# Optimization experiments

Measured on AMD Instinct MI355X. Metric: run time of the kernel, lower is better.

Reference implementation:

```python
import jax, jax.numpy as jnp
import numpy as np
import math

N, E, IN, OUT, H = 50000, 200000, 128, 128, 4
EPS = 1e-5
NEG_SLOPE = 0.01


def _ln(a):
    m = jnp.mean(a, axis=-1, keepdims=True)
    v = jnp.mean((a - m) ** 2, axis=-1, keepdims=True)
    return (a - m) / jnp.sqrt(v + EPS)


def setup_inputs() -> dict:
    key = jax.random.key(0)
    ks = jax.random.split(key, 24)
    glorot = lambda k, shape: jax.random.uniform(k, shape, jnp.float32,
                                                 -math.sqrt(6.0 / (shape[-2] + shape[-1])),
                                                 math.sqrt(6.0 / (shape[-2] + shape[-1])))
    lin = lambda k, fan_in, shape: jax.random.uniform(k, shape, jnp.float32,
                                                      -1.0 / math.sqrt(fan_in), 1.0 / math.sqrt(fan_in))
    inp = {
        "x": jax.random.normal(ks[0], (N, IN), jnp.float32),
        "edge_index": jax.random.randint(ks[1], (2, E), 0, N, jnp.int32),
        "edge_feature": jax.random.normal(ks[2], (E, IN), jnp.float32),
        # per-head projection matrices [H, IN, OUT]
        "Kv2v": glorot(ks[3], (H, IN, OUT)),
        "Ke2v": glorot(ks[4], (H, IN, OUT)),
        "Vv2v": glorot(ks[5], (H, IN, OUT)),
        "Ve2v": glorot(ks[6], (H, IN, OUT)),
        # per-head linear_update: [H, 2*OUT, 2*OUT]
        "lu_W": lin(ks[7], 2 * OUT, (H, 2 * OUT, 2 * OUT)),
        "lu_b": lin(ks[8], 2 * OUT, (H, 2 * OUT)),
        "ln1_g": jnp.ones((H, 2 * OUT), jnp.float32),
        "ln1_b": jnp.zeros((H, 2 * OUT), jnp.float32),
        # per-head msg_layer linear: [H, 2*OUT, OUT]
        "msg_W": lin(ks[9], 2 * OUT, (H, 2 * OUT, OUT)),
        "msg_b": lin(ks[10], 2 * OUT, (H, OUT)),
        "ln2_g": jnp.ones((H, OUT), jnp.float32),
        "ln2_b": jnp.zeros((H, OUT), jnp.float32),
        # concat projection [OUT*H, OUT]
        "cat_W": lin(ks[11], OUT * H, (OUT * H, OUT)),
        "cat_b": lin(ks[12], OUT * H, (OUT,)),
        # input projection [IN, OUT]
        "inp_W": lin(ks[13], IN, (IN, OUT)),
        "inp_b": lin(ks[14], IN, (OUT,)),
        # batchnorm affine
        "bn_g": jnp.ones((OUT,), jnp.float32),
        "bn_b": jnp.zeros((OUT,), jnp.float32),
    }
    return inp


def reference(x, edge_index, edge_feature, Kv2v, Ke2v, Vv2v, Ve2v,
              lu_W, lu_b, ln1_g, ln1_b, msg_W, msg_b, ln2_g, ln2_b,
              cat_W, cat_b, inp_W, inp_b, bn_g, bn_b):
    src, dst = edge_index[0], edge_index[1]  # j -> i
    scale = 1.0 / math.sqrt(2 * OUT)
    heads = []
    for h in range(H):  # small fixed loop over structurally distinct heads
        Kv = x @ Kv2v[h]            # [N, OUT]
        Vv = x @ Vv2v[h]
        KE = edge_feature @ Ke2v[h]  # [E, OUT]
        VE = edge_feature @ Ve2v[h]
        q_i = Kv[dst]                # [E, OUT]
        query = jnp.concatenate([q_i, q_i], axis=1)          # [E, 2*OUT]
        key_j = jnp.concatenate([Kv[src], KE], axis=1)       # [E, 2*OUT]
        alpha = query * key_j * scale
        val = jnp.concatenate([Vv[src], VE], axis=1)         # [E, 2*OUT]
        gate = jax.nn.sigmoid(_ln(alpha) * ln1_g[h] + ln1_b[h])
        m = (val @ lu_W[h] + lu_b[h]) * gate                 # [E, 2*OUT]
        m = m @ msg_W[h] + msg_b[h]                          # [E, OUT]
        m = _ln(m) * ln2_g[h] + ln2_b[h]
        m = jax.nn.leaky_relu(m, NEG_SLOPE)
        heads.append(jax.ops.segment_sum(m, dst, num_segments=N))  # [N, OUT]
    hv = jnp.concatenate(heads, axis=1)          # [N, OUT*H]
    out = hv @ cat_W + cat_b                      # [N, OUT]
    mu = jnp.mean(out, axis=0)
    var = jnp.mean((out - mu) ** 2, axis=0)      # biased, training-mode BN
    out = (out - mu) / jnp.sqrt(var + EPS) * bn_g + bn_b
    out = jax.nn.leaky_relu(out, NEG_SLOPE)
    return out + (x @ inp_W + inp_b)
```

## Files before the change

### kernel.cpp

```cpp
#include <hip/hip_runtime.h>
#include <hip/hip_bf16.h>

#define NN 50000
#define NE 200000
#define HEADS 4
#define EPSV 1e-5f
#define NEGS 0.01f

using f32x4 = __attribute__((ext_vector_type(4))) float;
using s16x8 = __attribute__((ext_vector_type(8))) short;
using bf16x8 = __attribute__((ext_vector_type(8))) __bf16;

__device__ __forceinline__ short f2bf(float f) {
    union { float f; unsigned u; } v; v.f = f;
    unsigned r = v.u + 0x7FFFu + ((v.u >> 16) & 1u);
    return (short)(r >> 16);
}
__device__ __forceinline__ float bf2f(short s) {
    union { unsigned u; float f; } v; v.u = ((unsigned)(unsigned short)s) << 16;
    return v.f;
}
__device__ __forceinline__ f32x4 mfma16(s16x8 a, s16x8 b, f32x4 c) {
    return __builtin_amdgcn_mfma_f32_16x16x32_bf16(
        __builtin_bit_cast(bf16x8, a), __builtin_bit_cast(bf16x8, b), c, 0, 0, 0);
}
__device__ __forceinline__ void gld16(const void* g, void* l) {
    __builtin_amdgcn_global_load_lds(
        (const __attribute__((address_space(1))) void*)g,
        (__attribute__((address_space(3))) void*)l, 16, 0, 0);
}
__device__ __forceinline__ void dma8(const short* src, char* dst, int w, int lane) {
    gld16(src + w * 512 + lane * 8,        dst + w * 1024);
    gld16(src + 2048 + w * 512 + lane * 8, dst + 4096 + w * 1024);
}

__global__ void prep_weights(const float* __restrict__ Kv2v, const float* __restrict__ Vv2v,
                             const float* __restrict__ inpW,
                             const float* __restrict__ Ke2v, const float* __restrict__ Ve2v,
                             const float* __restrict__ luW, const float* __restrict__ msgW,
                             const float* __restrict__ catW,
                             short* __restrict__ nodeW_t, short* __restrict__ imgW)
{
    int i = blockIdx.x * 256 + threadIdx.x;
    if (i < 147456) {
        int j = i >> 7, k = i & 127;
        float v;
        if (j < 512)       v = Kv2v[(j >> 7) * 16384 + k * 128 + (j & 127)];
        else if (j < 1024) v = Vv2v[((j - 512) >> 7) * 16384 + k * 128 + (j & 127)];
        else               v = inpW[k * 128 + (j - 1024)];
        nodeW_t[i] = f2bf(v);
        return;
    }
    i -= 147456;
    if (i >= 589824) return;
    int h = i / 147456;
    int r = i % 147456;
    short* img = imgW + h * 147456;
    if (r < 16384) {
        int colc = r >> 7, k = r & 127;
        img[(colc * 128 + k) ^ ((colc & 7) << 3)] = f2bf(Ke2v[h * 16384 + k * 128 + colc]);
    } else if (r < 32768) {
        int e = r - 16384; int colc = e >> 7, k = e & 127;
        img[16384 + ((colc * 128 + k) ^ ((colc & 7) << 3))] = f2bf(Ve2v[h * 16384 + k * 128 + colc]);
    } else if (r < 98304) {
        int e = r - 32768; int c = e >> 14, ec = e & 16383;
        int colc = ec >> 8, k = ec & 255; int col = c * 64 + colc;
        img[32768 + c * 16384 + ((colc * 256 + k) ^ ((colc & 7) << 3))] =
            f2bf(luW[h * 65536 + k * 256 + col]);
    } else if (r < 131072) {
        int e = r - 98304; int c = e >> 14, ec = e & 16383;
        int colc = ec >> 8, k = ec & 255; int col = c * 64 + colc;
        img[98304 + c * 16384 + ((colc * 256 + k) ^ ((colc & 7) << 3))] =
            f2bf(msgW[h * 32768 + k * 128 + col]);
    } else {
        int e = r - 131072; int colc = e >> 7, k = e & 127;
        img[131072 + ((colc * 128 + k) ^ ((colc & 7) << 3))] =
            f2bf(catW[(h * 128 + k) * 128 + colc]);
    }
}

__global__ __launch_bounds__(256, 2)
void node_proj(const float* __restrict__ x, const short* __restrict__ nodeW_t,
               short* __restrict__ Kv_all, short* __restrict__ Vv_all,
               float* __restrict__ resid)
{
    __shared__ alignas(16) short xt[64 * 128];
    const int tid = threadIdx.x;
    const int row0 = blockIdx.x * 64;
    #pragma unroll
    for (int it = 0; it < 8; ++it) {
        int idx4 = it * 256 + tid;
        int r = idx4 >> 5;
        int c = (idx4 & 31) * 4;
        float4 v = {0.f, 0.f, 0.f, 0.f};
        if (row0 + r < NN) v = *(const float4*)(x + (size_t)(row0 + r) * 128 + c);
        short4 sw; sw.x = f2bf(v.x); sw.y = f2bf(v.y); sw.z = f2bf(v.z); sw.w = f2bf(v.w);
        int byte = (r * 256 + c * 2) ^ ((r & 7) << 4);
        *(short4*)((char*)xt + byte) = sw;
    }
    __syncthreads();
    const int lane = tid & 63, w = tid >> 6;
    const int l15 = lane & 15, lg = lane >> 4;
    const int rloc = w * 16 + l15;
    s16x8 a[4];
    #pragma unroll
    for (int ks = 0; ks < 4; ++ks) {
        int byte = (rloc * 256 + (ks * 32 + lg * 8) * 2) ^ ((rloc & 7) << 4);
        a[ks] = *(const s16x8*)((const char*)xt + byte);
    }
    const int rowC = row0 + w * 16 + lg * 4;
    for (int nc = 0; nc < 18; ++nc) {
        f32x4 acc[4];
        s16x8 b[16];
        #pragma unroll
        for (int q = 0; q < 4; ++q) {
            acc[q] = (f32x4){0.f, 0.f, 0.f, 0.f};
            int j = (nc * 4 + q) * 16 + l15;
            #pragma unroll
            for (int ks = 0; ks < 4; ++ks)
                b[q * 4 + ks] = *(const s16x8*)(nodeW_t + j * 128 + ks * 32 + lg * 8);
        }
        #pragma unroll
        for (int q = 0; q < 4; ++q)
            #pragma unroll
            for (int ks = 0; ks < 4; ++ks)
                acc[q] = mfma16(a[ks], b[q * 4 + ks], acc[q]);
        #pragma unroll
        for (int q = 0; q < 4; ++q) {
            int j = (nc * 4 + q) * 16 + l15;
            #pragma unroll
            for (int r = 0; r < 4; ++r) {
                int row = rowC + r;
                if (row >= NN) continue;
                if (j < 512)       Kv_all[(size_t)row * 512 + j] = f2bf(acc[q][r]);
                else if (j < 1024) Vv_all[(size_t)row * 512 + (j - 512)] = f2bf(acc[q][r]);
                else               resid[(size_t)row * 128 + (j - 1024)] = acc[q][r];
            }
        }
    }
}

#define B128h(buf, ct, ks) \
    (*(const s16x8*)((const short*)(buf) + (((((ct) * 16 + l15) * 128) + (ks) * 32 + lg * 8) ^ ((l15 & 7) << 3))))
#define B256h(buf, ks) \
    (*(const s16x8*)((const short*)(buf) + ((l15 * 256 + (ks) * 32 + lg * 8) ^ ((l15 & 7) << 3))))
#define WAITV(N) asm volatile("s_waitcnt vmcnt(" #N ")" ::: "memory")
#define SBAR() do { __builtin_amdgcn_s_barrier(); __builtin_amdgcn_sched_barrier(0); } while (0)
#define PRIO1() __builtin_amdgcn_s_setprio(1)
#define PRIO0() __builtin_amdgcn_s_setprio(0)

__global__ __launch_bounds__(256, 1)
void edge_kernel(const float* __restrict__ ef, const int* __restrict__ eidx,
                 const short* __restrict__ Kv_all, const short* __restrict__ Vv_all,
                 const short* __restrict__ imgW,
                 const float* __restrict__ lu_b, const float* __restrict__ ln1_g,
                 const float* __restrict__ ln1_b, const float* __restrict__ msg_b,
                 const float* __restrict__ ln2_g, const float* __restrict__ ln2_b,
                 float* __restrict__ out1)
{
    extern __shared__ char lds[];
    const int tid = threadIdx.x;
    const int lane = tid & 63, w = tid >> 6;
    const int l15 = lane & 15, lg = lane >> 4;
    const int e0 = blockIdx.x * 64 + w * 16;
    const int rb = lg * 4;
    char* myscr = lds + 32768 + w * 12288;
    float* bls = (float*)(lds + 81920);
    const float scale = 0.0625f;

    {
        int j = tid;
        #pragma unroll
        for (int it = 0; it < 4; ++it, j += 256) {
            bls[j] = ln1_g[j]; bls[1024 + j] = ln1_b[j]; bls[2048 + j] = lu_b[j];
        }
        if (tid < 256) {
            bls[3072 + tid] = msg_b[tid];       bls[3072 + 256 + tid] = msg_b[256 + tid];
            bls[3584 + tid] = ln2_g[tid];       bls[3584 + 256 + tid] = ln2_g[256 + tid];
            bls[4096 + tid] = ln2_b[tid];       bls[4096 + 256 + tid] = ln2_b[256 + tid];
        }
        asm volatile("s_waitcnt lgkmcnt(0)" ::: "memory");
    }

    const float* efr = ef + (size_t)(e0 + l15) * 128 + lg * 8;
    s16x8 aef[4];
    #pragma unroll
    for (int ks = 0; ks < 4; ++ks) {
        float4 v0 = *(const float4*)(efr + ks * 32);
        float4 v1 = *(const float4*)(efr + ks * 32 + 4);
        s16x8 t;
        t[0] = f2bf(v0.x); t[1] = f2bf(v0.y); t[2] = f2bf(v0.z); t[3] = f2bf(v0.w);
        t[4] = f2bf(v1.x); t[5] = f2bf(v1.y); t[6] = f2bf(v1.z); t[7] = f2bf(v1.w);
        aef[ks] = t;
    }
    const int srcA = eidx[e0 + l15];
    int dstC[4];
    #pragma unroll
    for (int r = 0; r < 4; ++r) dstC[r] = eidx[NE + e0 + rb + r];
    const int gRow = lane >> 2;
    const int gChunk = lane & 3;
    const int dstG = eidx[NE + e0 + gRow];
    const int srcG = eidx[e0 + gRow];

    dma8(imgW,        lds,         w, lane);
    dma8(imgW + 4096, lds + 8192,  w, lane);
    dma8(imgW + 8192, lds + 16384, w, lane);

    f32x4 outc[8];
    #pragma unroll
    for (int nt = 0; nt < 8; ++nt) outc[nt] = (f32x4){0.f, 0.f, 0.f, 0.f};

    for (int h = 0; h < HEADS; ++h) {
        const short* hb = imgW + h * 147456;
        f32x4 accK[8];
        #pragma unroll
        for (int nt = 0; nt < 8; ++nt) accK[nt] = (f32x4){0, 0, 0, 0};
        s16x8 vvr[4];
        unsigned gpk[16][2];

        #pragma unroll
        for (int p = 0; p < 4; ++p) {
            WAITV(4); SBAR();
            dma8(hb + (p + 3) * 4096, lds + ((p + 3) & 3) * 8192, w, lane);
            const char* bA = lds + (p & 3) * 8192;
            PRIO1();
            #pragma unroll
            for (int ks = 0; ks < 4; ++ks) {
                accK[p * 2]     = mfma16(aef[ks], B128h(bA, 0, ks), accK[p * 2]);
                accK[p * 2 + 1] = mfma16(aef[ks], B128h(bA, 1, ks), accK[p * 2 + 1]);
            }
            PRIO0();
            if (p == 0) {
                #pragma unroll
                for (int j = 0; j < 4; ++j) {
                    s16x8 qv = *(const s16x8*)(Kv_all + (size_t)dstG * 512 + h * 128 + gChunk * 32 + j * 8);
                    s16x8 kv = *(const s16x8*)(Kv_all + (size_t)srcG * 512 + h * 128 + gChunk * 32 + j * 8);
                    int byte = gRow * 256 + ((((gChunk * 4 + j) * 16)) ^ ((gRow & 7) << 4));
                    *(s16x8*)(myscr + byte) = qv;
                    *(s16x8*)(myscr + 4096 + byte) = kv;
                }
            }
        }

        #pragma unroll
        for (int i = 0; i < 4; ++i) {
            const int p = 4 + i;
            WAITV(4); SBAR();
            dma8(hb + (p + 3) * 4096, lds + ((p + 3) & 3) * 8192, w, lane);
            const char* bA = lds + (p & 3) * 8192;
            f32x4 aV0 = (f32x4){0, 0, 0, 0}, aV1 = (f32x4){0, 0, 0, 0};
            PRIO1();
            #pragma unroll
            for (int ks = 0; ks < 4; ++ks) {
                aV0 = mfma16(aef[ks], B128h(bA, 0, ks), aV0);
                aV1 = mfma16(aef[ks], B128h(bA, 1, ks), aV1);
            }
            PRIO0();
            #pragma unroll
            for (int t = 0; t < 2; ++t) {
                f32x4 av = t ? aV1 : aV0;
                int c = (i * 2 + t) * 16 + l15;
                #pragma unroll
                for (int r = 0; r < 4; ++r) {
                    int row = rb + r;
                    int byte = 8192 + ((row * 256 + c * 2) ^ ((row & 7) << 4));
                    *(short*)(myscr + byte) = f2bf(av[r]);
                }
            }
            if (i == 0) {
                #pragma unroll
                for (int ks = 0; ks < 4; ++ks)
                    vvr[ks] = *(const s16x8*)(Vv_all + (size_t)srcA * 512 + h * 128 + ks * 32 + lg * 8);
            }
            if (i == 3) {
                #pragma unroll
                for (int r = 0; r < 4; ++r) {
                    const int i2r = rb + r;
                    const int swz = (i2r & 7) << 4;
                    float al[16];
                    float s = 0.f, s2 = 0.f;
                    #pragma unroll
                    for (int nt = 0; nt < 8; ++nt) {
                        int off = (i2r * 256 + nt * 32 + l15 * 2) ^ swz;
                        float q  = bf2f(*(const short*)(myscr + off));
                        float k1 = bf2f(*(const short*)(myscr + 4096 + off));
                        float alo = q * k1 * scale;
                        float ahi = q * accK[nt][r] * scale;
                        al[nt] = alo; al[nt + 8] = ahi;
                        s += alo + ahi; s2 += alo * alo + ahi * ahi;
                    }
                    #pragma unroll
                    for (int m = 1; m < 16; m <<= 1) { s += __shfl_xor(s, m); s2 += __shfl_xor(s2, m); }
                    float mean = s * (1.f / 256.f);
                    float var  = s2 * (1.f / 256.f) - mean * mean;
                    float rstd = rsqrtf(var + EPSV);
                    #pragma unroll
                    for (int i2 = 0; i2 < 16; ++i2) {
                        int c = i2 * 16 + l15;
                        float z = (al[i2] - mean) * rstd * bls[h * 256 + c] + bls[1024 + h * 256 + c];
                        float g = 1.f / (1.f + __expf(-z));
                        unsigned gb = (unsigned)(unsigned short)f2bf(g);
                        if ((r & 1) == 0) gpk[i2][r >> 1] = gb;
                        else              gpk[i2][r >> 1] |= gb << 16;
                    }
                }
            }
        }

        #pragma unroll
        for (int c = 0; c < 16; ++c) {
            const int p = 8 + c;
            WAITV(4); SBAR();
            dma8(hb + (p + 3) * 4096, lds + ((p + 3) & 3) * 8192, w, lane);
            const char* bA = lds + (p & 3) * 8192;
            f32x4 m1c = (f32x4){0, 0, 0, 0};
            PRIO1();
            #pragma unroll
            for (int ks = 0; ks < 8; ++ks) {
                s16x8 a;
                if (ks < 4) a = vvr[ks];
                else {
                    int byte = 8192 + ((l15 * 256 + ((ks - 4) * 32 + lg * 8) * 2) ^ ((l15 & 7) << 4));
                    a = *(const s16x8*)(myscr + byte);
                }
                m1c = mfma16(a, B256h(bA, ks), m1c);
            }
            PRIO0();
            {
                int col = c * 16 + l15;
                float bias = bls[2048 + h * 256 + col];
                #pragma unroll
                for (int r = 0; r < 4; ++r) {
                    float g = bf2f((short)((gpk[c][r >> 1] >> ((r & 1) * 16)) & 0xFFFFu));
                    int row = rb + r;
                    int byte = (row * 512 + col * 2) ^ ((row & 7) << 4);
                    *(short*)(myscr + byte) = f2bf((m1c[r] + bias) * g);
                }
            }
        }

        f32x4 m2[8];
        #pragma unroll
        for (int nt = 0; nt < 8; ++nt) m2[nt] = (f32x4){0, 0, 0, 0};
        #pragma unroll
        for (int c = 0; c < 8; ++c) {
            const int p = 24 + c;
            WAITV(4); SBAR();
            dma8(hb + (p + 3) * 4096, lds + ((p + 3) & 3) * 8192, w, lane);
            const char* bA = lds + (p & 3) * 8192;
            PRIO1();
            #pragma unroll
            for (int ks = 0; ks < 8; ++ks) {
                int byte = (l15 * 512 + (ks * 32 + lg * 8) * 2) ^ ((l15 & 7) << 4);
                s16x8 a = *(const s16x8*)(myscr + byte);
                m2[c] = mfma16(a, B256h(bA, ks), m2[c]);
            }
            PRIO0();
        }
        {
            float s[4] = {0, 0, 0, 0}, s2[4] = {0, 0, 0, 0};
            #pragma unroll
            for (int nt = 0; nt < 8; ++nt) {
                int c = nt * 16 + l15;
                float bias = bls[3072 + h * 128 + c];
                #pragma unroll
                for (int r = 0; r < 4; ++r) {
                    float v = m2[nt][r] + bias;
                    m2[nt][r] = v;
                    s[r] += v; s2[r] += v * v;
                }
            }
            #pragma unroll
            for (int m = 1; m < 16; m <<= 1)
                #pragma unroll
                for (int r = 0; r < 4; ++r) { s[r] += __shfl_xor(s[r], m); s2[r] += __shfl_xor(s2[r], m); }
            float mean[4], rstd[4];
            #pragma unroll
            for (int r = 0; r < 4; ++r) {
                mean[r] = s[r] * (1.f / 128.f);
                float var = s2[r] * (1.f / 128.f) - mean[r] * mean[r];
                rstd[r] = rsqrtf(var + EPSV);
            }
            #pragma unroll
            for (int nt = 0; nt < 8; ++nt) {
                int c = nt * 16 + l15;
                float g2 = bls[3584 + h * 128 + c], b2 = bls[4096 + h * 128 + c];
                #pragma unroll
                for (int r = 0; r < 4; ++r) {
                    float v = (m2[nt][r] - mean[r]) * rstd[r] * g2 + b2;
                    v = v > 0.f ? v : v * NEGS;
                    int row = rb + r;
                    int byte = 8192 + ((row * 256 + c * 2) ^ ((row & 7) << 4));
                    *(short*)(myscr + byte) = f2bf(v);
                }
            }
        }

        #pragma unroll
        for (int c = 0; c < 4; ++c) {
            const int p = 32 + c;
            if (p < 34)      { WAITV(4); }
            else if (p == 34) { if (h < 3) { WAITV(4); } else { WAITV(2); } }
            else              { if (h < 3) { WAITV(4); } else { WAITV(0); } }
            SBAR();
            const int t = p + 3;
            if (t < 36) {
                dma8(hb + t * 4096, lds + (t & 3) * 8192, w, lane);
            } else if (h < 3) {
                dma8(imgW + (h + 1) * 147456 + (t - 36) * 4096, lds + (t & 3) * 8192, w, lane);
            }
            const char* bA = lds + (p & 3) * 8192;
            PRIO1();
            #pragma unroll
            for (int ks = 0; ks < 4; ++ks) {
                int byte = 8192 + ((l15 * 256 + (ks * 32 + lg * 8) * 2) ^ ((l15 & 7) << 4));
                s16x8 a = *(const s16x8*)(myscr + byte);
                outc[c * 2]     = mfma16(a, B128h(bA, 0, ks), outc[c * 2]);
                outc[c * 2 + 1] = mfma16(a, B128h(bA, 1, ks), outc[c * 2 + 1]);
            }
            PRIO0();
        }
    }

    #pragma unroll
    for (int nt = 0; nt < 8; ++nt) {
        int c = nt * 16 + l15;
        #pragma unroll
        for (int r = 0; r < 4; ++r)
            atomicAdd(out1 + (size_t)dstC[r] * 128 + c, outc[nt][r]);
    }
}

__global__ void bn_stats(const float* __restrict__ out1, const float* __restrict__ cat_b,
                         float* __restrict__ stats)
{
    const int col = threadIdx.x;
    const int r0 = blockIdx.x * 128;
    const float cb = cat_b[col];
    float s = 0.f, s2 = 0.f;
    for (int i = 0; i < 128; ++i) {
        int row = r0 + i;
        if (row < NN) {
            float v = out1[(size_t)row * 128 + col] + cb;
            s += v; s2 += v * v;
        }
    }
    atomicAdd(stats + col, s);
    atomicAdd(stats + 128 + col, s2);
}

__global__ void finalize(const float* __restrict__ out1, const float* __restrict__ resid,
                         const float* __restrict__ stats, const float* __restrict__ cat_b,
                         const float* __restrict__ bn_g, const float* __restrict__ bn_b,
                         const float* __restrict__ inp_b, float* __restrict__ out)
{
    int i = blockIdx.x * 256 + threadIdx.x;
    if (i >= NN * 128) return;
    int col = i & 127;
    float mu = stats[col] * (1.f / NN);
    float var = stats[128 + col] * (1.f / NN) - mu * mu;
    float rstd = rsqrtf(var + EPSV);
    float v = out1[i] + cat_b[col];
    v = (v - mu) * rstd * bn_g[col] + bn_b[col];
    v = v > 0.f ? v : v * NEGS;
    out[i] = v + resid[i] + inp_b[col];
}

extern "C" void kernel_launch(void* const* d_in, const int* in_sizes, int n_in,
                              void* d_out, int out_size, void* d_ws, size_t ws_size,
                              hipStream_t stream)
{
    (void)in_sizes; (void)n_in; (void)out_size; (void)ws_size;
    const float* x     = (const float*)d_in[0];
    const int*   eidx  = (const int*)d_in[1];
    const float* ef    = (const float*)d_in[2];
    const float* Kv2v  = (const float*)d_in[3];
    const float* Ke2v  = (const float*)d_in[4];
    const float* Vv2v  = (const float*)d_in[5];
    const float* Ve2v  = (const float*)d_in[6];
    const float* lu_W  = (const float*)d_in[7];
    const float* lu_b  = (const float*)d_in[8];
    const float* ln1_g = (const float*)d_in[9];
    const float* ln1_b = (const float*)d_in[10];
    const float* msg_W = (const float*)d_in[11];
    const float* msg_b = (const float*)d_in[12];
    const float* ln2_g = (const float*)d_in[13];
    const float* ln2_b = (const float*)d_in[14];
    const float* cat_W = (const float*)d_in[15];
    const float* cat_b = (const float*)d_in[16];
    const float* inp_W = (const float*)d_in[17];
    const float* inp_b = (const float*)d_in[18];
    const float* bn_g  = (const float*)d_in[19];
    const float* bn_b  = (const float*)d_in[20];

    char* ws = (char*)d_ws;
    short* nodeW_t = (short*)(ws + 0);
    short* imgW    = (short*)(ws + 294912);
    short* Kv_all  = (short*)(ws + 1474560);
    short* Vv_all  = (short*)(ws + 52674560);
    float* resid   = (float*)(ws + 103874560);
    float* out1    = (float*)(ws + 129474560);
    float* stats   = (float*)(ws + 155074560);

    hipFuncSetAttribute((const void*)edge_kernel,
                        hipFuncAttributeMaxDynamicSharedMemorySize, 100352);

    hipMemsetAsync(out1, 0, 25600000 + 1024, stream);
    prep_weights<<<2880, 256, 0, stream>>>(Kv2v, Vv2v, inp_W, Ke2v, Ve2v, lu_W, msg_W, cat_W,
                                           nodeW_t, imgW);
    node_proj<<<782, 256, 0, stream>>>(x, nodeW_t, Kv_all, Vv_all, resid);
    edge_kernel<<<3125, 256, 100352, stream>>>(ef, eidx, Kv_all, Vv_all, imgW,
                                               lu_b, ln1_g, ln1_b, msg_b,
                                               ln2_g, ln2_b, out1);
    bn_stats<<<391, 128, 0, stream>>>(out1, cat_b, stats);
    finalize<<<25000, 256, 0, stream>>>(out1, resid, stats, cat_b, bn_g, bn_b, inp_b,
                                        (float*)d_out);
}
```

Before: 1.339 ms.

## Double weight-stage chunk size to halve pipeline barriers in edge kernel

The weight-streaming pipeline in the edge kernel now moves 16KB chunks per stage instead of 8KB, so there are 18 stages per head instead of 36. Each stage issues twice as many async global-to-LDS loads and does twice the MFMA work between barriers. Ring buffer slots use a per-head phase offset so the prefetch for the next head continues across head boundaries. This cuts barrier and wait overhead per head, at the cost of raising LDS use to about 130KB, which still fits at one block per CU.

```diff
diff --git a/kernel.cpp b/kernel.cpp
--- a/kernel.cpp
+++ b/kernel.cpp
@@ -29,9 +29,10 @@
         (const __attribute__((address_space(1))) void*)g,
         (__attribute__((address_space(3))) void*)l, 16, 0, 0);
 }
-__device__ __forceinline__ void dma8(const short* src, char* dst, int w, int lane) {
-    gld16(src + w * 512 + lane * 8,        dst + w * 1024);
-    gld16(src + 2048 + w * 512 + lane * 8, dst + 4096 + w * 1024);
+__device__ __forceinline__ void dma16(const short* src, char* dst, int w, int lane) {
+    #pragma unroll
+    for (int op = 0; op < 4; ++op)
+        gld16(src + op * 2048 + w * 512 + lane * 8, dst + op * 4096 + w * 1024);
 }
 
 __global__ void prep_weights(const float* __restrict__ Kv2v, const float* __restrict__ Vv2v,
@@ -142,12 +143,20 @@
 
 #define B128h(buf, ct, ks) \
     (*(const s16x8*)((const short*)(buf) + (((((ct) * 16 + l15) * 128) + (ks) * 32 + lg * 8) ^ ((l15 & 7) << 3))))
-#define B256h(buf, ks) \
-    (*(const s16x8*)((const short*)(buf) + ((l15 * 256 + (ks) * 32 + lg * 8) ^ ((l15 & 7) << 3))))
+#define B256h(buf, tt, ks) \
+    (*(const s16x8*)((const short*)(buf) + (((((tt) * 16 + l15) * 256) + (ks) * 32 + lg * 8) ^ ((l15 & 7) << 3))))
 #define WAITV(N) asm volatile("s_waitcnt vmcnt(" #N ")" ::: "memory")
 #define SBAR() do { __builtin_amdgcn_s_barrier(); __builtin_amdgcn_sched_barrier(0); } while (0)
 #define PRIO1() __builtin_amdgcn_s_setprio(1)
 #define PRIO0() __builtin_amdgcn_s_setprio(0)
+#define STEP_SYNC(s) do { \
+    if (h < 3 || (s) < 16) { WAITV(8); } \
+    else if ((s) == 16)    { WAITV(4); } \
+    else                   { WAITV(0); } \
+    SBAR(); \
+    if ((s) <= 14)      dma16(hb + ((s) + 3) * 8192, lds + ((ph + (s) + 3) & 3) * 16384, w, lane); \
+    else if (h < 3)     dma16(hbn + ((s) - 15) * 8192, lds + ((ph + (s) + 3) & 3) * 16384, w, lane); \
+} while (0)
 
 __global__ __launch_bounds__(256, 1)
 void edge_kernel(const float* __restrict__ ef, const int* __restrict__ eidx,
@@ -164,8 +173,8 @@
     const int l15 = lane & 15, lg = lane >> 4;
     const int e0 = blockIdx.x * 64 + w * 16;
     const int rb = lg * 4;
-    char* myscr = lds + 32768 + w * 12288;
-    float* bls = (float*)(lds + 81920);
+    char* myscr = lds + 65536 + w * 12288;
+    float* bls = (float*)(lds + 114688);
     const float scale = 0.0625f;
 
     {
@@ -174,11 +183,9 @@
         for (int it = 0; it < 4; ++it, j += 256) {
             bls[j] = ln1_g[j]; bls[1024 + j] = ln1_b[j]; bls[2048 + j] = lu_b[j];
         }
-        if (tid < 256) {
-            bls[3072 + tid] = msg_b[tid];       bls[3072 + 256 + tid] = msg_b[256 + tid];
-            bls[3584 + tid] = ln2_g[tid];       bls[3584 + 256 + tid] = ln2_g[256 + tid];
-            bls[4096 + tid] = ln2_b[tid];       bls[4096 + 256 + tid] = ln2_b[256 + tid];
-        }
+        bls[3072 + tid] = msg_b[tid];   bls[3072 + 256 + tid] = msg_b[256 + tid];
+        bls[3584 + tid] = ln2_g[tid];   bls[3584 + 256 + tid] = ln2_g[256 + tid];
+        bls[4096 + tid] = ln2_b[tid];   bls[4096 + 256 + tid] = ln2_b[256 + tid];
         asm volatile("s_waitcnt lgkmcnt(0)" ::: "memory");
     }
 
@@ -202,16 +209,18 @@
     const int dstG = eidx[NE + e0 + gRow];
     const int srcG = eidx[e0 + gRow];
 
-    dma8(imgW,        lds,         w, lane);
-    dma8(imgW + 4096, lds + 8192,  w, lane);
-    dma8(imgW + 8192, lds + 16384, w, lane);
+    dma16(imgW,         lds,          w, lane);
+    dma16(imgW + 8192,  lds + 16384,  w, lane);
+    dma16(imgW + 16384, lds + 32768,  w, lane);
 
     f32x4 outc[8];
     #pragma unroll
     for (int nt = 0; nt < 8; ++nt) outc[nt] = (f32x4){0.f, 0.f, 0.f, 0.f};
 
     for (int h = 0; h < HEADS; ++h) {
-        const short* hb = imgW + h * 147456;
+        const short* hb  = imgW + h * 147456;
+        const short* hbn = imgW + (h + 1) * 147456;
+        const int ph = (h & 1) * 2;
         f32x4 accK[8];
         #pragma unroll
         for (int nt = 0; nt < 8; ++nt) accK[nt] = (f32x4){0, 0, 0, 0};
@@ -219,18 +228,17 @@
         unsigned gpk[16][2];
 
         #pragma unroll
-        for (int p = 0; p < 4; ++p) {
-            WAITV(4); SBAR();
-            dma8(hb + (p + 3) * 4096, lds + ((p + 3) & 3) * 8192, w, lane);
-            const char* bA = lds + (p & 3) * 8192;
+        for (int s = 0; s < 2; ++s) {
+            STEP_SYNC(s);
+            const char* bA = lds + ((ph + s) & 3) * 16384;
             PRIO1();
             #pragma unroll
-            for (int ks = 0; ks < 4; ++ks) {
-                accK[p * 2]     = mfma16(aef[ks], B128h(bA, 0, ks), accK[p * 2]);
-                accK[p * 2 + 1] = mfma16(aef[ks], B128h(bA, 1, ks), accK[p * 2 + 1]);
-            }
+            for (int ks = 0; ks < 4; ++ks)
+                #pragma unroll
+                for (int ct = 0; ct < 4; ++ct)
+                    accK[s * 4 + ct] = mfma16(aef[ks], B128h(bA, ct, ks), accK[s * 4 + ct]);
             PRIO0();
-            if (p == 0) {
+            if (s == 0) {
                 #pragma unroll
                 for (int j = 0; j < 4; ++j) {
                     s16x8 qv = *(const s16x8*)(Kv_all + (size_t)dstG * 512 + h * 128 + gChunk * 32 + j * 8);
@@ -243,28 +251,28 @@
         }
 
         #pragma unroll
-        for (int i = 0; i < 4; ++i) {
-            const int p = 4 + i;
-            WAITV(4); SBAR();
-            dma8(hb + (p + 3) * 4096, lds + ((p + 3) & 3) * 8192, w, lane);
-            const char* bA = lds + (p & 3) * 8192;
-            f32x4 aV0 = (f32x4){0, 0, 0, 0}, aV1 = (f32x4){0, 0, 0, 0};
+        for (int i = 0; i < 2; ++i) {
+            const int s = 2 + i;
+            STEP_SYNC(s);
+            const char* bA = lds + ((ph + s) & 3) * 16384;
+            f32x4 aV[4];
+            #pragma unroll
+            for (int t = 0; t < 4; ++t) aV[t] = (f32x4){0, 0, 0, 0};
             PRIO1();
             #pragma unroll
-            for (int ks = 0; ks < 4; ++ks) {
-                aV0 = mfma16(aef[ks], B128h(bA, 0, ks), aV0);
-                aV1 = mfma16(aef[ks], B128h(bA, 1, ks), aV1);
-            }
+            for (int ks = 0; ks < 4; ++ks)
+                #pragma unroll
+                for (int t = 0; t < 4; ++t)
+                    aV[t] = mfma16(aef[ks], B128h(bA, t, ks), aV[t]);
             PRIO0();
             #pragma unroll
-            for (int t = 0; t < 2; ++t) {
-                f32x4 av = t ? aV1 : aV0;
-                int c = (i * 2 + t) * 16 + l15;
+            for (int t = 0; t < 4; ++t) {
+                int c = (i * 4 + t) * 16 + l15;
                 #pragma unroll
                 for (int r = 0; r < 4; ++r) {
                     int row = rb + r;
                     int byte = 8192 + ((row * 256 + c * 2) ^ ((row & 7) << 4));
-                    *(short*)(myscr + byte) = f2bf(av[r]);
+                    *(short*)(myscr + byte) = f2bf(aV[t][r]);
                 }
             }
             if (i == 0) {
@@ -272,13 +280,13 @@
                 for (int ks = 0; ks < 4; ++ks)
                     vvr[ks] = *(const s16x8*)(Vv_all + (size_t)srcA * 512 + h * 128 + ks * 32 + lg * 8);
             }
-            if (i == 3) {
+            if (i == 1) {
                 #pragma unroll
                 for (int r = 0; r < 4; ++r) {
                     const int i2r = rb + r;
                     const int swz = (i2r & 7) << 4;
                     float al[16];
-                    float s = 0.f, s2 = 0.f;
+                    float s1 = 0.f, s2 = 0.f;
                     #pragma unroll
                     for (int nt = 0; nt < 8; ++nt) {
                         int off = (i2r * 256 + nt * 32 + l15 * 2) ^ swz;
@@ -287,11 +295,11 @@
                         float alo = q * k1 * scale;
                         float ahi = q * accK[nt][r] * scale;
                         al[nt] = alo; al[nt + 8] = ahi;
-                        s += alo + ahi; s2 += alo * alo + ahi * ahi;
+                        s1 += alo + ahi; s2 += alo * alo + ahi * ahi;
                     }
                     #pragma unroll
-                    for (int m = 1; m < 16; m <<= 1) { s += __shfl_xor(s, m); s2 += __shfl_xor(s2, m); }
-                    float mean = s * (1.f / 256.f);
+                    for (int m = 1; m < 16; m <<= 1) { s1 += __shfl_xor(s1, m); s2 += __shfl_xor(s2, m); }
+                    float mean = s1 * (1.f / 256.f);
                     float var  = s2 * (1.f / 256.f) - mean * mean;
                     float rstd = rsqrtf(var + EPSV);
                     #pragma unroll
@@ -308,30 +316,31 @@
         }
 
         #pragma unroll
-        for (int c = 0; c < 16; ++c) {
-            const int p = 8 + c;
-            WAITV(4); SBAR();
-            dma8(hb + (p + 3) * 4096, lds + ((p + 3) & 3) * 8192, w, lane);
-            const char* bA = lds + (p & 3) * 8192;
-            f32x4 m1c = (f32x4){0, 0, 0, 0};
-            PRIO1();
-            #pragma unroll
-            for (int ks = 0; ks < 8; ++ks) {
-                s16x8 a;
-                if (ks < 4) a = vvr[ks];
-                else {
-                    int byte = 8192 + ((l15 * 256 + ((ks - 4) * 32 + lg * 8) * 2) ^ ((l15 & 7) << 4));
-                    a = *(const s16x8*)(myscr + byte);
-                }
-                m1c = mfma16(a, B256h(bA, ks), m1c);
-            }
-            PRIO0();
-            {
-                int col = c * 16 + l15;
+        for (int c = 0; c < 8; ++c) {
+            const int s = 4 + c;
+            STEP_SYNC(s);
+            const char* bA = lds + ((ph + s) & 3) * 16384;
+            #pragma unroll
+            for (int tt = 0; tt < 2; ++tt) {
+                const int cidx = c * 2 + tt;
+                f32x4 m1c = (f32x4){0, 0, 0, 0};
+                PRIO1();
+                #pragma unroll
+                for (int ks = 0; ks < 8; ++ks) {
+                    s16x8 a;
+                    if (ks < 4) a = vvr[ks];
+                    else {
+                        int byte = 8192 + ((l15 * 256 + ((ks - 4) * 32 + lg * 8) * 2) ^ ((l15 & 7) << 4));
+                        a = *(const s16x8*)(myscr + byte);
+                    }
+                    m1c = mfma16(a, B256h(bA, tt, ks), m1c);
+                }
+                PRIO0();
+                int col = cidx * 16 + l15;
                 float bias = bls[2048 + h * 256 + col];
                 #pragma unroll
                 for (int r = 0; r < 4; ++r) {
-                    float g = bf2f((short)((gpk[c][r >> 1] >> ((r & 1) * 16)) & 0xFFFFu));
+                    float g = bf2f((short)((gpk[cidx][r >> 1] >> ((r & 1) * 16)) & 0xFFFFu));
                     int row = rb + r;
                     int byte = (row * 512 + col * 2) ^ ((row & 7) << 4);
                     *(short*)(myscr + byte) = f2bf((m1c[r] + bias) * g);
@@ -343,22 +352,22 @@
         #pragma unroll
         for (int nt = 0; nt < 8; ++nt) m2[nt] = (f32x4){0, 0, 0, 0};
         #pragma unroll
-        for (int c = 0; c < 8; ++c) {
-            const int p = 24 + c;
-            WAITV(4); SBAR();
-            dma8(hb + (p + 3) * 4096, lds + ((p + 3) & 3) * 8192, w, lane);
-            const char* bA = lds + (p & 3) * 8192;
+        for (int c = 0; c < 4; ++c) {
+            const int s = 12 + c;
+            STEP_SYNC(s);
+            const char* bA = lds + ((ph + s) & 3) * 16384;
             PRIO1();
             #pragma unroll
             for (int ks = 0; ks < 8; ++ks) {
                 int byte = (l15 * 512 + (ks * 32 + lg * 8) * 2) ^ ((l15 & 7) << 4);
                 s16x8 a = *(const s16x8*)(myscr + byte);
-                m2[c] = mfma16(a, B256h(bA, ks), m2[c]);
+                m2[c * 2]     = mfma16(a, B256h(bA, 0, ks), m2[c * 2]);
+                m2[c * 2 + 1] = mfma16(a, B256h(bA, 1, ks), m2[c * 2 + 1]);
             }
             PRIO0();
         }
         {
-            float s[4] = {0, 0, 0, 0}, s2[4] = {0, 0, 0, 0};
+            float s1[4] = {0, 0, 0, 0}, s2[4] = {0, 0, 0, 0};
             #pragma unroll
             for (int nt = 0; nt < 8; ++nt) {
                 int c = nt * 16 + l15;
@@ -367,17 +376,17 @@
                 for (int r = 0; r < 4; ++r) {
                     float v = m2[nt][r] + bias;
                     m2[nt][r] = v;
-                    s[r] += v; s2[r] += v * v;
+                    s1[r] += v; s2[r] += v * v;
                 }
             }
             #pragma unroll
             for (int m = 1; m < 16; m <<= 1)
                 #pragma unroll
-                for (int r = 0; r < 4; ++r) { s[r] += __shfl_xor(s[r], m); s2[r] += __shfl_xor(s2[r], m); }
+                for (int r = 0; r < 4; ++r) { s1[r] += __shfl_xor(s1[r], m); s2[r] += __shfl_xor(s2[r], m); }
             float mean[4], rstd[4];
             #pragma unroll
             for (int r = 0; r < 4; ++r) {
-                mean[r] = s[r] * (1.f / 128.f);
+                mean[r] = s1[r] * (1.f / 128.f);
                 float var = s2[r] * (1.f / 128.f) - mean[r] * mean[r];
                 rstd[r] = rsqrtf(var + EPSV);
             }
@@ -397,26 +406,18 @@
         }
 
         #pragma unroll
-        for (int c = 0; c < 4; ++c) {
-            const int p = 32 + c;
-            if (p < 34)      { WAITV(4); }
-            else if (p == 34) { if (h < 3) { WAITV(4); } else { WAITV(2); } }
-            else              { if (h < 3) { WAITV(4); } else { WAITV(0); } }
-            SBAR();
-            const int t = p + 3;
-            if (t < 36) {
-                dma8(hb + t * 4096, lds + (t & 3) * 8192, w, lane);
-            } else if (h < 3) {
-                dma8(imgW + (h + 1) * 147456 + (t - 36) * 4096, lds + (t & 3) * 8192, w, lane);
-            }
-            const char* bA = lds + (p & 3) * 8192;
+        for (int c = 0; c < 2; ++c) {
+            const int s = 16 + c;
+            STEP_SYNC(s);
+            const char* bA = lds + ((ph + s) & 3) * 16384;
             PRIO1();
             #pragma unroll
             for (int ks = 0; ks < 4; ++ks) {
                 int byte = 8192 + ((l15 * 256 + (ks * 32 + lg * 8) * 2) ^ ((l15 & 7) << 4));
                 s16x8 a = *(const s16x8*)(myscr + byte);
-                outc[c * 2]     = mfma16(a, B128h(bA, 0, ks), outc[c * 2]);
-                outc[c * 2 + 1] = mfma16(a, B128h(bA, 1, ks), outc[c * 2 + 1]);
+                #pragma unroll
+                for (int ct = 0; ct < 4; ++ct)
+                    outc[c * 4 + ct] = mfma16(a, B128h(bA, ct, ks), outc[c * 4 + ct]);
             }
             PRIO0();
         }
@@ -503,13 +504,13 @@
     float* stats   = (float*)(ws + 155074560);
 
     hipFuncSetAttribute((const void*)edge_kernel,
-                        hipFuncAttributeMaxDynamicSharedMemorySize, 100352);
+                        hipFuncAttributeMaxDynamicSharedMemorySize, 133120);
 
     hipMemsetAsync(out1, 0, 25600000 + 1024, stream);
     prep_weights<<<2880, 256, 0, stream>>>(Kv2v, Vv2v, inp_W, Ke2v, Ve2v, lu_W, msg_W, cat_W,
                                            nodeW_t, imgW);
     node_proj<<<782, 256, 0, stream>>>(x, nodeW_t, Kv_all, Vv_all, resid);
-    edge_kernel<<<3125, 256, 100352, stream>>>(ef, eidx, Kv_all, Vv_all, imgW,
+    edge_kernel<<<3125, 256, 133120, stream>>>(ef, eidx, Kv_all, Vv_all, imgW,
                                                lu_b, ln1_g, ln1_b, msg_b,
                                                ln2_g, ln2_b, out1);
     bn_stats<<<391, 128, 0, stream>>>(out1, cat_b, stats);
```

After: 1.373 ms. 2.5% more time.
